# Kernel tuning notes

Hardware: AMD Instinct MI355X
Metric: run time of the kernel (lower is better)

The kernel has to match this reference:

```python
import jax, jax.numpy as jnp
import numpy as np

N_NODES = 100001      # total_nodes + 1
N_EDGES = 6400000     # avg degree ~64
LATENT_DIM = 32
N_LAYERS = 2


def setup_inputs() -> dict:
    key = jax.random.key(0)
    k1, k2, k3, k4 = jax.random.split(key, 4)
    emb_weight = jax.random.normal(k1, (N_NODES, LATENT_DIM), dtype=jnp.float32) * 0.1
    adj_vals = jax.random.uniform(k2, (N_EDGES,), dtype=jnp.float32)
    adj_row = jax.random.randint(k3, (N_EDGES,), 0, N_NODES, dtype=jnp.int32)
    adj_col = jax.random.randint(k4, (N_EDGES,), 0, N_NODES, dtype=jnp.int32)
    return {"emb_weight": emb_weight, "adj_vals": adj_vals,
            "adj_row": adj_row, "adj_col": adj_col}


def reference(emb_weight, adj_vals, adj_row, adj_col):
    n = emb_weight.shape[0]

    def spmm(x):
        # y[r] = sum_{e: row[e]==r} vals[e] * x[col[e]]  (torch.sparse.mm COO)
        gathered = adj_vals[:, None] * x[adj_col]  # [E, D]
        return jax.ops.segment_sum(gathered, adj_row, num_segments=n)

    emb = emb_weight
    acc = emb                      # layer-0 embedding
    for _ in range(N_LAYERS):
        emb = spmm(emb)
        acc = acc + emb
    # mean over (n_layers + 1) stacked embeddings
    return acc / jnp.float32(N_LAYERS + 1)
```

## Files before the change

kernel.cpp:

```cpp
#include <hip/hip_runtime.h>


constexpr int D = 32;
constexpr int RPB_LOG = 8;
constexpr int RPB = 1 << RPB_LOG;
constexpr int MAXNB = 512;
constexpr int TILE = 4096;
constexpr int PT2 = 512;
constexpr int CAP = 9728;
constexpr float QSCALE = 32768.0f;
constexpr float QINV = 1.0f / 32768.0f;

__device__ __forceinline__ unsigned short f2bf(float f) {
    unsigned u = __float_as_uint(f);
    unsigned r = (u + 0x7FFFu + ((u >> 16) & 1u)) >> 16;
    return (unsigned short)r;
}
__device__ __forceinline__ float bf2f(unsigned short h) {
    return __uint_as_float((unsigned)h << 16);
}
__device__ __forceinline__ float lo_f(unsigned v) {
    return __uint_as_float(v << 16);
}
__device__ __forceinline__ float hi_f(unsigned v) {
    return __uint_as_float(v & 0xFFFF0000u);
}

__global__ void zero_f32(float* __restrict__ p, int n) {
    int i = blockIdx.x * blockDim.x + threadIdx.x;
    if (i < n) p[i] = 0.0f;
}
__global__ void cast_bf16(const float* __restrict__ in,
                          unsigned short* __restrict__ out, int n) {
    int i = blockIdx.x * blockDim.x + threadIdx.x;
    if (i < n) out[i] = f2bf(in[i]);
}

__global__ __launch_bounds__(256) void tile_hist(
    const int* __restrict__ row, int* __restrict__ tileCnt, int nE, int NB) {
    __shared__ int h[MAXNB];
    int tile = blockIdx.x;
    int base = tile * TILE;
    int n = min(TILE, nE - base);
    int t = threadIdx.x;
    for (int i = t; i < NB; i += 256) h[i] = 0;
    __syncthreads();
    for (int i = t; i < n; i += 256)
        atomicAdd(&h[row[base + i] >> RPB_LOG], 1);
    __syncthreads();
    for (int i = t; i < NB; i += 256)
        tileCnt[(size_t)tile * NB + i] = h[i];
}

__global__ __launch_bounds__(256) void colscan(
    int* __restrict__ tileCnt, int* __restrict__ cnt, int nTiles, int NB) {
    __shared__ int s2[256];
    __shared__ int carryS;
    int b = blockIdx.x, t = threadIdx.x;
    if (t == 0) carryS = 0;
    __syncthreads();
    for (int c0 = 0; c0 < nTiles; c0 += 1024) {
        int v[4], idx[4];
        int sum = 0;
#pragma unroll
        for (int k = 0; k < 4; ++k) {
            idx[k] = c0 + t * 4 + k;
            v[k] = (idx[k] < nTiles) ? tileCnt[(size_t)idx[k] * NB + b] : 0;
            sum += v[k];
        }
        s2[t] = sum;
        __syncthreads();
        for (int o = 1; o < 256; o <<= 1) {
            int x = (t >= o) ? s2[t - o] : 0;
            __syncthreads();
            s2[t] += x;
            __syncthreads();
        }
        int run = ((t == 0) ? 0 : s2[t - 1]) + carryS;
#pragma unroll
        for (int k = 0; k < 4; ++k) {
            if (idx[k] < nTiles) tileCnt[(size_t)idx[k] * NB + b] = run;
            run += v[k];
        }
        __syncthreads();
        if (t == 0) carryS += s2[255];
        __syncthreads();
    }
    if (t == 0) cnt[b] = carryS;
}

__global__ __launch_bounds__(512) void scan_buckets(
    const int* __restrict__ cnt, int* __restrict__ bases, int NB, int nE) {
    __shared__ int s[MAXNB];
    int t = threadIdx.x;
    s[t] = (t < NB) ? cnt[t] : 0;
    __syncthreads();
    for (int o = 1; o < 512; o <<= 1) {
        int v = (t >= o) ? s[t - o] : 0;
        __syncthreads();
        s[t] += v;
        __syncthreads();
    }
    if (t < NB) bases[t] = (t == 0) ? 0 : s[t - 1];
    if (t == 0) bases[NB] = nE;
}

__global__ __launch_bounds__(PT2) void partition_edges2(
    const int* __restrict__ row, const int* __restrict__ col,
    const float* __restrict__ vals, const int* __restrict__ bases,
    const int* __restrict__ tileCnt, uint2* __restrict__ cv, int nE, int NB) {
    __shared__ uint2 buf[TILE];
    __shared__ unsigned short bkt[TILE];
    __shared__ int hist[MAXNB];
    __shared__ int runoff[MAXNB];
    __shared__ int s2[PT2];
    int t = threadIdx.x;
    int tile = blockIdx.x;
    int base = tile * TILE;
    int n = min(TILE, nE - base);
    if (n <= 0) return;
    for (int i = t; i < NB; i += PT2) hist[i] = 0;
    __syncthreads();
    for (int i = t; i < n; i += PT2)
        atomicAdd(&hist[row[base + i] >> RPB_LOG], 1);
    __syncthreads();
    {
        int a0 = (t < NB) ? hist[t] : 0;
        s2[t] = a0;
        __syncthreads();
        for (int o = 1; o < PT2; o <<= 1) {
            int v = (t >= o) ? s2[t - o] : 0;
            __syncthreads();
            s2[t] += v;
            __syncthreads();
        }
        if (t < NB) runoff[t] = s2[t] - a0;
    }
    __syncthreads();
    for (int i = t; i < NB; i += PT2)
        hist[i] = bases[i] + tileCnt[(size_t)tile * NB + i] - runoff[i];
    __syncthreads();
    for (int i = t; i < n; i += PT2) {
        int r = row[base + i];
        int b = r >> RPB_LOG;
        int slot = atomicAdd(&runoff[b], 1);
        float v = vals[base + i];
        int q = __float2int_rn(v * QSCALE);
        q = max(0, min(32767, q));
        uint2 p;
        p.x = (unsigned)col[base + i] | ((unsigned)(r & (RPB - 1)) << 17);
        p.y = (unsigned)q;
        buf[slot] = p;
        bkt[slot] = (unsigned short)b;
    }
    __syncthreads();
    for (int i = t; i < n; i += PT2)
        cv[hist[bkt[i]] + i] = buf[i];
}

__global__ __launch_bounds__(512) void csr_sort4(
    const int* __restrict__ bases, const uint2* __restrict__ cv,
    unsigned* __restrict__ cv2, int* __restrict__ rowptr, int n, int nE) {
    __shared__ unsigned stage[CAP];
    __shared__ int hist_s[RPB];
    __shared__ int cur_s[RPB];
    int t = threadIdx.x;
    int b = blockIdx.x >> 1;
    int h = blockIdx.x & 1;
    int s = bases[b], e = bases[b + 1];
    if (t < RPB) hist_s[t] = 0;
    __syncthreads();
    for (int i = s + t; i < e; i += 512)
        atomicAdd(&hist_s[cv[i].x >> 17], 1);
    __syncthreads();
    if (t < RPB) cur_s[t] = hist_s[t];
    __syncthreads();
    for (int o = 1; o < RPB; o <<= 1) {
        int v = 0;
        if (t < RPB && t >= o) v = cur_s[t - o];
        __syncthreads();
        if (t < RPB) cur_s[t] += v;
        __syncthreads();
    }
    int excl = 0;
    if (t < RPB) excl = (t == 0) ? 0 : cur_s[t - 1];
    int half_lo = h << 7;
    __syncthreads();
    int base_h = (half_lo == 0) ? 0 : cur_s[half_lo - 1];
    int end_h  = cur_s[half_lo + 127];
    int cnt_h  = end_h - base_h;
    __syncthreads();
    if (t < RPB) {
        if ((t >> 7) == h) {
            int r = (b << RPB_LOG) + t;
            if (r < n) rowptr[r] = s + excl;
            cur_s[t] = excl - base_h;
        }
    }
    if (b == 0 && h == 0 && t == 0) rowptr[n] = nE;
    __syncthreads();
    bool fits = (cnt_h <= CAP);
    for (int i = s + t; i < e; i += 512) {
        uint2 p = cv[i];
        int r = (int)(p.x >> 17);
        if ((r >> 7) != h) continue;
        int slot = atomicAdd(&cur_s[r], 1);
        unsigned packed = (p.x & 0x1FFFFu) | (p.y << 17);
        if (fits) stage[slot] = packed;
        else      cv2[s + base_h + slot] = packed;
    }
    __syncthreads();
    if (fits) {
        int dst = s + base_h;
        for (int j = t; j < cnt_h; j += 512)
            cv2[dst + j] = stage[j];
    }
}

__global__ __launch_bounds__(256) void spmm_l1(
    const int* __restrict__ ptr, const unsigned* __restrict__ cv,
    const unsigned* __restrict__ xd, unsigned* __restrict__ yd, int nRows) {
    int g = (blockIdx.x * 256 + threadIdx.x) >> 4;
    if (g >= nRows) return;
    int lane = threadIdx.x & 15;
    int e = ptr[g], end = ptr[g + 1];
    float a0 = 0.0f, a1 = 0.0f;
    for (; e + 8 <= end; e += 8) {
        unsigned q0 = cv[e], q1 = cv[e + 1], q2 = cv[e + 2], q3 = cv[e + 3];
        unsigned q4 = cv[e + 4], q5 = cv[e + 5], q6 = cv[e + 6], q7 = cv[e + 7];
        unsigned v0 = xd[(size_t)(q0 & 0x1FFFFu) * 16 + lane];
        unsigned v1 = xd[(size_t)(q1 & 0x1FFFFu) * 16 + lane];
        unsigned v2 = xd[(size_t)(q2 & 0x1FFFFu) * 16 + lane];
        unsigned v3 = xd[(size_t)(q3 & 0x1FFFFu) * 16 + lane];
        unsigned v4 = xd[(size_t)(q4 & 0x1FFFFu) * 16 + lane];
        unsigned v5 = xd[(size_t)(q5 & 0x1FFFFu) * 16 + lane];
        unsigned v6 = xd[(size_t)(q6 & 0x1FFFFu) * 16 + lane];
        unsigned v7 = xd[(size_t)(q7 & 0x1FFFFu) * 16 + lane];
        float s0 = (float)(q0 >> 17), s1 = (float)(q1 >> 17);
        float s2 = (float)(q2 >> 17), s3 = (float)(q3 >> 17);
        float s4 = (float)(q4 >> 17), s5 = (float)(q5 >> 17);
        float s6 = (float)(q6 >> 17), s7 = (float)(q7 >> 17);
        a0 += s0 * lo_f(v0);  a1 += s0 * hi_f(v0);
        a0 += s1 * lo_f(v1);  a1 += s1 * hi_f(v1);
        a0 += s2 * lo_f(v2);  a1 += s2 * hi_f(v2);
        a0 += s3 * lo_f(v3);  a1 += s3 * hi_f(v3);
        a0 += s4 * lo_f(v4);  a1 += s4 * hi_f(v4);
        a0 += s5 * lo_f(v5);  a1 += s5 * hi_f(v5);
        a0 += s6 * lo_f(v6);  a1 += s6 * hi_f(v6);
        a0 += s7 * lo_f(v7);  a1 += s7 * hi_f(v7);
    }
    for (; e < end; ++e) {
        unsigned q = cv[e];
        unsigned v = xd[(size_t)(q & 0x1FFFFu) * 16 + lane];
        float s = (float)(q >> 17);
        a0 += s * lo_f(v);
        a1 += s * hi_f(v);
    }
    unsigned packed = (unsigned)f2bf(a0 * QINV) |
                      ((unsigned)f2bf(a1 * QINV) << 16);
    yd[(size_t)g * 16 + lane] = packed;
}

__global__ __launch_bounds__(256) void spmm_combine(
    const int* __restrict__ ptr, const unsigned* __restrict__ cv,
    const unsigned* __restrict__ yd, const float2* __restrict__ emb2,
    float2* __restrict__ out2, int nRows) {
    int g = (blockIdx.x * 256 + threadIdx.x) >> 4;
    if (g >= nRows) return;
    int lane = threadIdx.x & 15;
    int e = ptr[g], end = ptr[g + 1];
    float a0 = 0.0f, a1 = 0.0f;
    for (; e + 8 <= end; e += 8) {
        unsigned q0 = cv[e], q1 = cv[e + 1], q2 = cv[e + 2], q3 = cv[e + 3];
        unsigned q4 = cv[e + 4], q5 = cv[e + 5], q6 = cv[e + 6], q7 = cv[e + 7];
        unsigned v0 = yd[(size_t)(q0 & 0x1FFFFu) * 16 + lane];
        unsigned v1 = yd[(size_t)(q1 & 0x1FFFFu) * 16 + lane];
        unsigned v2 = yd[(size_t)(q2 & 0x1FFFFu) * 16 + lane];
        unsigned v3 = yd[(size_t)(q3 & 0x1FFFFu) * 16 + lane];
        unsigned v4 = yd[(size_t)(q4 & 0x1FFFFu) * 16 + lane];
        unsigned v5 = yd[(size_t)(q5 & 0x1FFFFu) * 16 + lane];
        unsigned v6 = yd[(size_t)(q6 & 0x1FFFFu) * 16 + lane];
        unsigned v7 = yd[(size_t)(q7 & 0x1FFFFu) * 16 + lane];
        float s0 = (float)(q0 >> 17), s1 = (float)(q1 >> 17);
        float s2 = (float)(q2 >> 17), s3 = (float)(q3 >> 17);
        float s4 = (float)(q4 >> 17), s5 = (float)(q5 >> 17);
        float s6 = (float)(q6 >> 17), s7 = (float)(q7 >> 17);
        a0 += s0 * lo_f(v0);  a1 += s0 * hi_f(v0);
        a0 += s1 * lo_f(v1);  a1 += s1 * hi_f(v1);
        a0 += s2 * lo_f(v2);  a1 += s2 * hi_f(v2);
        a0 += s3 * lo_f(v3);  a1 += s3 * hi_f(v3);
        a0 += s4 * lo_f(v4);  a1 += s4 * hi_f(v4);
        a0 += s5 * lo_f(v5);  a1 += s5 * hi_f(v5);
        a0 += s6 * lo_f(v6);  a1 += s6 * hi_f(v6);
        a0 += s7 * lo_f(v7);  a1 += s7 * hi_f(v7);
    }
    for (; e < end; ++e) {
        unsigned q = cv[e];
        unsigned v = yd[(size_t)(q & 0x1FFFFu) * 16 + lane];
        float s = (float)(q >> 17);
        a0 += s * lo_f(v);
        a1 += s * hi_f(v);
    }
    size_t idx = (size_t)g * 16 + lane;
    float2 eb = emb2[idx];
    unsigned yv = yd[idx];
    float2 r;
    r.x = (eb.x + lo_f(yv) + a0 * QINV) * (1.0f / 3.0f);
    r.y = (eb.y + hi_f(yv) + a1 * QINV) * (1.0f / 3.0f);
    out2[idx] = r;
}

__global__ __launch_bounds__(256) void spmm_atomic(
    const int* __restrict__ row, const int* __restrict__ col,
    const float* __restrict__ vals, const float* __restrict__ x,
    float* __restrict__ y, int nEdges, float scale) {
    long long t = (long long)blockIdx.x * blockDim.x + threadIdx.x;
    int e = (int)(t >> 5);
    if (e >= nEdges) return;
    int d = (int)(t & 31);
    float g = vals[e] * scale * x[(long long)col[e] * D + d];
    atomicAdd(&y[(long long)row[e] * D + d], g);
}
__global__ void combine_third(const float* __restrict__ emb,
                              const float* __restrict__ y1,
                              float* __restrict__ out, int n) {
    int i = blockIdx.x * blockDim.x + threadIdx.x;
    if (i < n) out[i] = (emb[i] + y1[i]) * (1.0f / 3.0f);
}

extern "C" void kernel_launch(void* const* d_in, const int* in_sizes, int n_in,
                              void* d_out, int out_size, void* d_ws, size_t ws_size,
                              hipStream_t stream) {
    const float* emb  = (const float*)d_in[0];
    const float* vals = (const float*)d_in[1];
    const int*   row  = (const int*)d_in[2];
    const int*   col  = (const int*)d_in[3];
    float* out = (float*)d_out;

    const int nElem  = in_sizes[0];
    const int nEdges = in_sizes[1];
    const int n      = nElem / D;
    const int NB     = (n + RPB - 1) >> RPB_LOG;
    const int BLK = 256;
    const int nTiles = (nEdges + TILE - 1) / TILE;

    size_t off_cnt    = 0;
    size_t off_bases  = off_cnt + (size_t)NB * 4;
    size_t off_rowptr = off_bases + (size_t)(NB + 1) * 4;
    size_t off_cv     = (off_rowptr + (size_t)(n + 1) * 4 + 63) & ~(size_t)63;
    size_t off_cv2    = off_cv + (size_t)nEdges * 8;
    size_t need       = off_cv2 + (size_t)nEdges * 4;

    bool aliasFit   = ((size_t)nElem * 4 <= (size_t)nEdges * 8);
    bool tileCntFit = ((size_t)nTiles * NB * 4 <= (size_t)nEdges * 4);
    bool ok = (NB <= MAXNB) && (n <= 131072) && (ws_size >= need) &&
              aliasFit && tileCntFit;

    if (!ok) {
        if (ws_size < (size_t)nElem * 4) return;
        float* y1 = (float*)d_ws;
        zero_f32<<<(nElem + BLK - 1) / BLK, BLK, 0, stream>>>(y1, nElem);
        long long threads = (long long)nEdges * 32;
        int blocks = (int)((threads + BLK - 1) / BLK);
        spmm_atomic<<<blocks, BLK, 0, stream>>>(row, col, vals, emb, y1, nEdges, 1.0f);
        combine_third<<<(nElem + BLK - 1) / BLK, BLK, 0, stream>>>(emb, y1, out, nElem);
        spmm_atomic<<<blocks, BLK, 0, stream>>>(row, col, vals, y1, out, nEdges, 1.0f / 3.0f);
        return;
    }

    char* ws = (char*)d_ws;
    int*            cnt     = (int*)(ws + off_cnt);
    int*            bases   = (int*)(ws + off_bases);
    int*            rowptr  = (int*)(ws + off_rowptr);
    uint2*          cv      = (uint2*)(ws + off_cv);
    unsigned*       cv2     = (unsigned*)(ws + off_cv2);
    int*            tileCnt = (int*)(ws + off_cv2);
    unsigned*       yd      = (unsigned*)(ws + off_cv);
    unsigned short* embh    = (unsigned short*)(ws + off_cv + (size_t)nElem * 2);
    unsigned*       xd      = (unsigned*)embh;

    tile_hist<<<nTiles, 256, 0, stream>>>(row, tileCnt, nEdges, NB);

    colscan<<<NB, 256, 0, stream>>>(tileCnt, cnt, nTiles, NB);

    scan_buckets<<<1, 512, 0, stream>>>(cnt, bases, NB, nEdges);

    partition_edges2<<<nTiles, PT2, 0, stream>>>(row, col, vals, bases,
                                                 tileCnt, cv, nEdges, NB);

    csr_sort4<<<2 * NB, 512, 0, stream>>>(bases, cv, cv2, rowptr, n, nEdges);

    cast_bf16<<<(nElem + BLK - 1) / BLK, BLK, 0, stream>>>(emb, embh, nElem);

    int rowBlocks = (n * 16 + BLK - 1) / BLK;
    spmm_l1<<<rowBlocks, BLK, 0, stream>>>(rowptr, cv2, xd, yd, n);

    spmm_combine<<<rowBlocks, BLK, 0, stream>>>(rowptr, cv2, yd,
                                                (const float2*)emb,
                                                (float2*)out, n);
}
```

Baseline: 249.4 us.

## Split SpMM gathers into two column-half passes for cache locality

```diff
diff --git a/kernel.cpp b/kernel.cpp
--- a/kernel.cpp
+++ b/kernel.cpp
@@ -4,10 +4,11 @@
 constexpr int D = 32;
 constexpr int RPB_LOG = 8;
 constexpr int RPB = 1 << RPB_LOG;
+constexpr int KEYS = 2 * RPB;
 constexpr int MAXNB = 512;
 constexpr int TILE = 4096;
 constexpr int PT2 = 512;
-constexpr int CAP = 9728;
+constexpr int CAP = 9216;
 constexpr float QSCALE = 32768.0f;
 constexpr float QINV = 1.0f / 32768.0f;
 
@@ -15,9 +16,6 @@
     unsigned u = __float_as_uint(f);
     unsigned r = (u + 0x7FFFu + ((u >> 16) & 1u)) >> 16;
     return (unsigned short)r;
-}
-__device__ __forceinline__ float bf2f(unsigned short h) {
-    return __uint_as_float((unsigned)h << 16);
 }
 __device__ __forceinline__ float lo_f(unsigned v) {
     return __uint_as_float(v << 16);
@@ -110,7 +108,6 @@
     const float* __restrict__ vals, const int* __restrict__ bases,
     const int* __restrict__ tileCnt, uint2* __restrict__ cv, int nE, int NB) {
     __shared__ uint2 buf[TILE];
-    __shared__ unsigned short bkt[TILE];
     __shared__ int hist[MAXNB];
     __shared__ int runoff[MAXNB];
     __shared__ int s2[PT2];
@@ -149,63 +146,66 @@
         q = max(0, min(32767, q));
         uint2 p;
         p.x = (unsigned)col[base + i] | ((unsigned)(r & (RPB - 1)) << 17);
-        p.y = (unsigned)q;
+        p.y = (unsigned)q | ((unsigned)b << 15);
         buf[slot] = p;
-        bkt[slot] = (unsigned short)b;
-    }
-    __syncthreads();
-    for (int i = t; i < n; i += PT2)
-        cv[hist[bkt[i]] + i] = buf[i];
-}
-
-__global__ __launch_bounds__(512) void csr_sort4(
+    }
+    __syncthreads();
+    for (int i = t; i < n; i += PT2) {
+        uint2 v = buf[i];
+        cv[hist[v.y >> 15] + i] = v;
+    }
+}
+
+__global__ __launch_bounds__(512) void csr_sort5(
     const int* __restrict__ bases, const uint2* __restrict__ cv,
-    unsigned* __restrict__ cv2, int* __restrict__ rowptr, int n, int nE) {
+    unsigned* __restrict__ cv2, int* __restrict__ rowptr2,
+    int n, int nE, int half) {
     __shared__ unsigned stage[CAP];
-    __shared__ int hist_s[RPB];
-    __shared__ int cur_s[RPB];
+    __shared__ int hist_s[KEYS];
+    __shared__ int cur_s[KEYS];
     int t = threadIdx.x;
     int b = blockIdx.x >> 1;
     int h = blockIdx.x & 1;
     int s = bases[b], e = bases[b + 1];
-    if (t < RPB) hist_s[t] = 0;
-    __syncthreads();
-    for (int i = s + t; i < e; i += 512)
-        atomicAdd(&hist_s[cv[i].x >> 17], 1);
-    __syncthreads();
-    if (t < RPB) cur_s[t] = hist_s[t];
-    __syncthreads();
-    for (int o = 1; o < RPB; o <<= 1) {
-        int v = 0;
-        if (t < RPB && t >= o) v = cur_s[t - o];
-        __syncthreads();
-        if (t < RPB) cur_s[t] += v;
-        __syncthreads();
-    }
-    int excl = 0;
-    if (t < RPB) excl = (t == 0) ? 0 : cur_s[t - 1];
-    int half_lo = h << 7;
-    __syncthreads();
-    int base_h = (half_lo == 0) ? 0 : cur_s[half_lo - 1];
-    int end_h  = cur_s[half_lo + 127];
+    hist_s[t] = 0;
+    __syncthreads();
+    for (int i = s + t; i < e; i += 512) {
+        uint2 p = cv[i];
+        int key = (int)((p.x >> 17) << 1) |
+                  (((int)(p.x & 0x1FFFFu) >= half) ? 1 : 0);
+        atomicAdd(&hist_s[key], 1);
+    }
+    __syncthreads();
+    cur_s[t] = hist_s[t];
+    __syncthreads();
+    for (int o = 1; o < KEYS; o <<= 1) {
+        int v = (t >= o) ? cur_s[t - o] : 0;
+        __syncthreads();
+        cur_s[t] += v;
+        __syncthreads();
+    }
+    int excl = (t == 0) ? 0 : cur_s[t - 1];
+    __syncthreads();
+    int kh = h << 8;
+    int base_h = (kh == 0) ? 0 : cur_s[kh - 1];
+    int end_h  = cur_s[kh + 255];
     int cnt_h  = end_h - base_h;
     __syncthreads();
-    if (t < RPB) {
-        if ((t >> 7) == h) {
-            int r = (b << RPB_LOG) + t;
-            if (r < n) rowptr[r] = s + excl;
-            cur_s[t] = excl - base_h;
-        }
-    }
-    if (b == 0 && h == 0 && t == 0) rowptr[n] = nE;
+    if ((t >> 8) == h) {
+        int r = (b << RPB_LOG) + (t >> 1);
+        if (r < n) rowptr2[((size_t)r << 1) | (t & 1)] = s + excl;
+        cur_s[t] = excl - base_h;
+    }
+    if (b == 0 && h == 0 && t == 0) rowptr2[2 * n] = nE;
     __syncthreads();
     bool fits = (cnt_h <= CAP);
     for (int i = s + t; i < e; i += 512) {
         uint2 p = cv[i];
-        int r = (int)(p.x >> 17);
-        if ((r >> 7) != h) continue;
-        int slot = atomicAdd(&cur_s[r], 1);
-        unsigned packed = (p.x & 0x1FFFFu) | (p.y << 17);
+        int key = (int)((p.x >> 17) << 1) |
+                  (((int)(p.x & 0x1FFFFu) >= half) ? 1 : 0);
+        if ((key >> 8) != h) continue;
+        int slot = atomicAdd(&cur_s[key], 1);
+        unsigned packed = (p.x & 0x1FFFFu) | ((p.y & 0x7FFFu) << 17);
         if (fits) stage[slot] = packed;
         else      cv2[s + base_h + slot] = packed;
     }
@@ -217,13 +217,15 @@
     }
 }
 
+template <int PHASE>
 __global__ __launch_bounds__(256) void spmm_l1(
-    const int* __restrict__ ptr, const unsigned* __restrict__ cv,
-    const unsigned* __restrict__ xd, unsigned* __restrict__ yd, int nRows) {
+    const int* __restrict__ ptr2, const unsigned* __restrict__ cv,
+    const unsigned* __restrict__ xd, float2* __restrict__ part,
+    unsigned* __restrict__ yd, int nRows) {
     int g = (blockIdx.x * 256 + threadIdx.x) >> 4;
     if (g >= nRows) return;
     int lane = threadIdx.x & 15;
-    int e = ptr[g], end = ptr[g + 1];
+    int e = ptr2[2 * g + PHASE], end = ptr2[2 * g + PHASE + 1];
     float a0 = 0.0f, a1 = 0.0f;
     for (; e + 8 <= end; e += 8) {
         unsigned q0 = cv[e], q1 = cv[e + 1], q2 = cv[e + 2], q3 = cv[e + 3];
@@ -256,19 +258,26 @@
         a0 += s * lo_f(v);
         a1 += s * hi_f(v);
     }
-    unsigned packed = (unsigned)f2bf(a0 * QINV) |
-                      ((unsigned)f2bf(a1 * QINV) << 16);
-    yd[(size_t)g * 16 + lane] = packed;
-}
-
-__global__ __launch_bounds__(256) void spmm_combine(
-    const int* __restrict__ ptr, const unsigned* __restrict__ cv,
+    size_t idx = (size_t)g * 16 + lane;
+    if (PHASE == 0) {
+        part[idx] = make_float2(a0, a1);
+    } else {
+        float2 p = part[idx];
+        unsigned packed = (unsigned)f2bf((p.x + a0) * QINV) |
+                          ((unsigned)f2bf((p.y + a1) * QINV) << 16);
+        yd[idx] = packed;
+    }
+}
+
+template <int PHASE>
+__global__ __launch_bounds__(256) void spmm_l2(
+    const int* __restrict__ ptr2, const unsigned* __restrict__ cv,
     const unsigned* __restrict__ yd, const float2* __restrict__ emb2,
-    float2* __restrict__ out2, int nRows) {
+    float2* __restrict__ part, float2* __restrict__ out2, int nRows) {
     int g = (blockIdx.x * 256 + threadIdx.x) >> 4;
     if (g >= nRows) return;
     int lane = threadIdx.x & 15;
-    int e = ptr[g], end = ptr[g + 1];
+    int e = ptr2[2 * g + PHASE], end = ptr2[2 * g + PHASE + 1];
     float a0 = 0.0f, a1 = 0.0f;
     for (; e + 8 <= end; e += 8) {
         unsigned q0 = cv[e], q1 = cv[e + 1], q2 = cv[e + 2], q3 = cv[e + 3];
@@ -302,12 +311,17 @@
         a1 += s * hi_f(v);
     }
     size_t idx = (size_t)g * 16 + lane;
-    float2 eb = emb2[idx];
-    unsigned yv = yd[idx];
-    float2 r;
-    r.x = (eb.x + lo_f(yv) + a0 * QINV) * (1.0f / 3.0f);
-    r.y = (eb.y + hi_f(yv) + a1 * QINV) * (1.0f / 3.0f);
-    out2[idx] = r;
+    if (PHASE == 0) {
+        part[idx] = make_float2(a0, a1);
+    } else {
+        float2 eb = emb2[idx];
+        unsigned yv = yd[idx];
+        float2 p = part[idx];
+        float2 r;
+        r.x = (eb.x + lo_f(yv) + (p.x + a0) * QINV) * (1.0f / 3.0f);
+        r.y = (eb.y + hi_f(yv) + (p.y + a1) * QINV) * (1.0f / 3.0f);
+        out2[idx] = r;
+    }
 }
 
 __global__ __launch_bounds__(256) void spmm_atomic(
@@ -343,15 +357,16 @@
     const int NB     = (n + RPB - 1) >> RPB_LOG;
     const int BLK = 256;
     const int nTiles = (nEdges + TILE - 1) / TILE;
+    const int half   = n / 2;
 
     size_t off_cnt    = 0;
     size_t off_bases  = off_cnt + (size_t)NB * 4;
     size_t off_rowptr = off_bases + (size_t)(NB + 1) * 4;
-    size_t off_cv     = (off_rowptr + (size_t)(n + 1) * 4 + 63) & ~(size_t)63;
+    size_t off_cv     = (off_rowptr + (size_t)(2 * n + 1) * 4 + 63) & ~(size_t)63;
     size_t off_cv2    = off_cv + (size_t)nEdges * 8;
     size_t need       = off_cv2 + (size_t)nEdges * 4;
 
-    bool aliasFit   = ((size_t)nElem * 4 <= (size_t)nEdges * 8);
+    bool aliasFit   = ((size_t)nElem * 8 <= (size_t)nEdges * 8);
     bool tileCntFit = ((size_t)nTiles * NB * 4 <= (size_t)nEdges * 4);
     bool ok = (NB <= MAXNB) && (n <= 131072) && (ws_size >= need) &&
               aliasFit && tileCntFit;
@@ -371,13 +386,14 @@
     char* ws = (char*)d_ws;
     int*            cnt     = (int*)(ws + off_cnt);
     int*            bases   = (int*)(ws + off_bases);
-    int*            rowptr  = (int*)(ws + off_rowptr);
+    int*            rowptr2 = (int*)(ws + off_rowptr);
     uint2*          cv      = (uint2*)(ws + off_cv);
     unsigned*       cv2     = (unsigned*)(ws + off_cv2);
     int*            tileCnt = (int*)(ws + off_cv2);
     unsigned*       yd      = (unsigned*)(ws + off_cv);
     unsigned short* embh    = (unsigned short*)(ws + off_cv + (size_t)nElem * 2);
     unsigned*       xd      = (unsigned*)embh;
+    float2*         part    = (float2*)(ws + off_cv + (size_t)nElem * 4);
 
     tile_hist<<<nTiles, 256, 0, stream>>>(row, tileCnt, nEdges, NB);
 
@@ -388,14 +404,19 @@
     partition_edges2<<<nTiles, PT2, 0, stream>>>(row, col, vals, bases,
                                                  tileCnt, cv, nEdges, NB);
 
-    csr_sort4<<<2 * NB, 512, 0, stream>>>(bases, cv, cv2, rowptr, n, nEdges);
+    csr_sort5<<<2 * NB, 512, 0, stream>>>(bases, cv, cv2, rowptr2,
+                                          n, nEdges, half);
 
     cast_bf16<<<(nElem + BLK - 1) / BLK, BLK, 0, stream>>>(emb, embh, nElem);
 
     int rowBlocks = (n * 16 + BLK - 1) / BLK;
-    spmm_l1<<<rowBlocks, BLK, 0, stream>>>(rowptr, cv2, xd, yd, n);
-
-    spmm_combine<<<rowBlocks, BLK, 0, stream>>>(rowptr, cv2, yd,
-                                                (const float2*)emb,
-                                                (float2*)out, n);
-}
+    spmm_l1<0><<<rowBlocks, BLK, 0, stream>>>(rowptr2, cv2, xd, part, yd, n);
+    spmm_l1<1><<<rowBlocks, BLK, 0, stream>>>(rowptr2, cv2, xd, part, yd, n);
+
+    spmm_l2<0><<<rowBlocks, BLK, 0, stream>>>(rowptr2, cv2, yd,
+                                              (const float2*)emb, part,
+                                              (float2*)out, n);
+    spmm_l2<1><<<rowBlocks, BLK, 0, stream>>>(rowptr2, cv2, yd,
+                                              (const float2*)emb, part,
+                                              (float2*)out, n);
+}
```

Result: no change. 246.5 us (-1.1%).
